# Kernel optimization log

Measured on AMD Instinct MI355X. Metric: run time of the kernel, lower is better.

The kernel has to match this reference:

```python
import jax, jax.numpy as jnp
import numpy as np

B, S, D, H, MULT = 4, 2048, 768, 12, 4
HD = D // H
EPS = 1e-6


def _ln(x, g, b):
    mu = jnp.mean(x, axis=-1, keepdims=True)
    var = jnp.var(x, axis=-1, keepdims=True)
    return (x - mu) * jax.lax.rsqrt(var + EPS) * g + b


def setup_inputs() -> dict:
    key = jax.random.key(0)
    ks = jax.random.split(key, 12)
    sd = 0.02
    inp = {
        "x": jax.random.normal(ks[0], (B, S, D), dtype=jnp.float32),
        "mask": jnp.ones((B, 1, 1, S), dtype=jnp.int32),
        "Wq": jax.random.normal(ks[1], (D, D), dtype=jnp.float32) * sd,
        "bq": jnp.zeros((D,), dtype=jnp.float32),
        "Wk": jax.random.normal(ks[2], (D, D), dtype=jnp.float32) * sd,
        "bk": jnp.zeros((D,), dtype=jnp.float32),
        "Wv": jax.random.normal(ks[3], (D, D), dtype=jnp.float32) * sd,
        "bv": jnp.zeros((D,), dtype=jnp.float32),
        "Wo": jax.random.normal(ks[4], (D, D), dtype=jnp.float32) * sd,
        "bo": jnp.zeros((D,), dtype=jnp.float32),
        "W1": jax.random.normal(ks[5], (D, MULT * D), dtype=jnp.float32) * sd,
        "b1": jnp.zeros((MULT * D,), dtype=jnp.float32),
        "W2": jax.random.normal(ks[6], (MULT * D, D), dtype=jnp.float32) * sd,
        "b2": jnp.zeros((D,), dtype=jnp.float32),
        "g1": jnp.ones((D,), dtype=jnp.float32),
        "be1": jnp.zeros((D,), dtype=jnp.float32),
        "g2": jnp.ones((D,), dtype=jnp.float32),
        "be2": jnp.zeros((D,), dtype=jnp.float32),
    }
    return inp


def reference(x, mask, Wq, bq, Wk, bk, Wv, bv, Wo, bo, W1, b1, W2, b2, g1, be1, g2, be2):
    scale = HD ** -0.5
    # projections -> [B,H,S,HD]
    q = (x @ Wq + bq).reshape(B, S, H, HD).transpose(0, 2, 1, 3)
    k = (x @ Wk + bk).reshape(B, S, H, HD).transpose(0, 2, 1, 3)
    v = (x @ Wv + bv).reshape(B, S, H, HD).transpose(0, 2, 1, 3)
    scores = jnp.einsum("bhqd,bhkd->bhqk", q, k) * scale
    scores = jnp.where(mask == 0, -jnp.inf, scores)
    attn = jax.nn.softmax(scores, axis=-1)
    out = jnp.einsum("bhqk,bhkd->bhqd", attn, v)
    out = out.transpose(0, 2, 1, 3).reshape(B, S, D)
    mha = out @ Wo + bo
    # residual + LN
    h = _ln(mha + x, g1, be1)
    # FFN (dropout inactive in eval; GELU exact as torch nn.GELU default)
    ff = jax.nn.gelu(h @ W1 + b1, approximate=False) @ W2 + b2
    return _ln(ff + h, g2, be2)
```

## Files before the change

kernel.cpp:

```cpp
#include <hip/hip_runtime.h>
#include <hip/hip_bf16.h>
#include <math.h>

#define B_  4
#define S_  2048
#define D_  768
#define H_  12
#define HD_ 64
#define DF_ 3072
#define BS_ (B_*S_)

#define QSCALE 0.18033688011112042f

typedef __attribute__((ext_vector_type(8))) short short8;
typedef __attribute__((ext_vector_type(4))) float f32x4;
typedef __attribute__((ext_vector_type(4))) int  int4v;

__device__ __forceinline__ unsigned short f2b(float f){
    unsigned int x = __float_as_uint(f);
    return (unsigned short)((x + 0x7fffu + ((x >> 16) & 1u)) >> 16);
}
__device__ __forceinline__ float b2f(unsigned short u){
    return __uint_as_float(((unsigned int)u) << 16);
}

typedef __attribute__((address_space(1))) void gvoid_t;
typedef __attribute__((address_space(3))) void lvoid_t;
__device__ __forceinline__ void gload_lds16(const unsigned short* g, unsigned short* l){
    __builtin_amdgcn_global_load_lds((gvoid_t*)g, (lvoid_t*)l, 16, 0, 0);
}

__global__ __launch_bounds__(256) void prep_kernel(
    const float* __restrict__ x,
    const float* __restrict__ Wq, const float* __restrict__ Wk,
    const float* __restrict__ Wv, const float* __restrict__ Wo,
    const float* __restrict__ W1, const float* __restrict__ W2,
    const float* __restrict__ bq, const float* __restrict__ bk, const float* __restrict__ bv,
    unsigned short* __restrict__ xb, unsigned short* __restrict__ wqkvT,
    unsigned short* __restrict__ woT, unsigned short* __restrict__ w1T,
    unsigned short* __restrict__ w2T, float* __restrict__ bqkv)
{
    const int NCVT = (BS_*D_)/256;
    int bid = blockIdx.x;
    if (bid < NCVT){
        int i = bid*256 + threadIdx.x;
        xb[i] = f2b(x[i]);
        return;
    }
    bid -= NCVT;
    __shared__ float t[32][33];
    const float* src; unsigned short* dst; int K, N, bx, by;
    if (bid < 4*576){
        int wsel = bid / 576, tt = bid % 576;
        bx = tt % 24; by = tt / 24; K = D_; N = D_;
        src = (wsel==0)?Wq:(wsel==1)?Wk:(wsel==2)?Wv:Wo;
        dst = (wsel<3) ? (wqkvT + (size_t)wsel*D_*D_) : woT;
    } else if (bid < 4*576 + 2304){
        int tt = bid - 4*576; bx = tt % 96; by = tt / 96; K = D_; N = DF_; src = W1; dst = w1T;
    } else if (bid < 4*576 + 2*2304){
        int tt = bid - 4*576 - 2304; bx = tt % 24; by = tt / 24; K = DF_; N = D_; src = W2; dst = w2T;
    } else {
        int i = (bid - (4*576 + 2*2304))*256 + threadIdx.x;
        if (i < 3*D_) bqkv[i] = (i < D_) ? bq[i] : (i < 2*D_) ? bk[i-D_] : bv[i-2*D_];
        return;
    }
    int tx = threadIdx.x & 31, ty = threadIdx.x >> 5;
    #pragma unroll
    for (int i = 0; i < 4; ++i)
        t[ty + i*8][tx] = src[(size_t)(by*32 + ty + i*8) * N + bx*32 + tx];
    __syncthreads();
    #pragma unroll
    for (int i = 0; i < 4; ++i)
        dst[(size_t)(bx*32 + ty + i*8) * K + by*32 + tx] = f2b(t[tx][ty + i*8]);
}

__global__ __launch_bounds__(256, 3) void gemm_tn(
    const unsigned short* __restrict__ A,
    const unsigned short* __restrict__ Bt,
    const float* __restrict__ bias,
    float* __restrict__ Cf,
    unsigned short* __restrict__ Cb,
    unsigned short* __restrict__ vtg,
    int M, int N, int K, int klen, int act)
{
    __shared__ __align__(16) unsigned short As[128*64];
    __shared__ __align__(16) unsigned short Bs[128*64];

    const int tid  = threadIdx.x;
    const int bm   = blockIdx.y, bn = blockIdx.x, bz = blockIdx.z;
    const int w    = tid >> 6, lane = tid & 63;
    const int l16  = lane & 15, quad = lane >> 4;
    const int wm   = (w >> 1) * 64, wn = (w & 1) * 64;
    const int kbeg = bz * klen;

    const unsigned short* Abase = A  + (size_t)bm * 128 * K;
    const unsigned short* Bbase = Bt + (size_t)bn * 128 * K;

    f32x4 acc[4][4] = {};

    for (int kt = kbeg; kt < kbeg + klen; kt += 64){
        #pragma unroll
        for (int c0 = 0; c0 < 4; ++c0){
            int c = tid + c0 * 256;
            int row = c >> 3, q = c & 7;
            int sw = (q ^ row) & 7;
            gload_lds16(Abase + (size_t)row * K + kt + sw*8, As + c*8);
            gload_lds16(Bbase + (size_t)row * K + kt + sw*8, Bs + c*8);
        }
        __syncthreads();

        #pragma unroll
        for (int kc = 0; kc < 2; ++kc){
            short8 af[4], bf[4];
            #pragma unroll
            for (int mi = 0; mi < 4; ++mi)
                af[mi] = *(const short8*)&As[(wm + mi*16 + l16)*64 + (((kc*4 + quad) ^ l16) & 7)*8];
            #pragma unroll
            for (int ni = 0; ni < 4; ++ni)
                bf[ni] = *(const short8*)&Bs[(wn + ni*16 + l16)*64 + (((kc*4 + quad) ^ l16) & 7)*8];
            #pragma unroll
            for (int mi = 0; mi < 4; ++mi)
                #pragma unroll
                for (int ni = 0; ni < 4; ++ni)
                    acc[mi][ni] = __builtin_amdgcn_mfma_f32_16x16x32_bf16(af[mi], bf[ni], acc[mi][ni], 0, 0, 0);
        }
        __syncthreads();
    }

    if (act == 2 && bn >= 12){
        #pragma unroll
        for (int mi = 0; mi < 4; ++mi){
            int rowbase = bm*128 + wm + mi*16 + quad*4;
            int bidx = rowbase >> 11, s0 = rowbase & 2047;
            int sp = (s0 & ~31) | (((s0 >> 2) & 3) << 3) | (((s0 >> 4) & 1) << 2);
            #pragma unroll
            for (int ni = 0; ni < 4; ++ni){
                int col  = bn*128 + wn + ni*16 + l16;
                int hcol = col - 2*D_;
                int hh   = hcol >> 6, dd = hcol & 63;
                float bia = bias ? bias[col] : 0.f;
                unsigned long long pk = 0;
                #pragma unroll
                for (int r = 0; r < 4; ++r)
                    pk |= (unsigned long long)f2b(acc[mi][ni][r] + bia) << (16*r);
                *(unsigned long long*)(vtg + (((size_t)bidx*H_ + hh)*64 + dd)*2048 + sp) = pk;
            }
        }
        return;
    }

    float* Cfz = Cf ? (Cf + (size_t)bz * M * N) : nullptr;
    const bool addb = (bias != nullptr) && (bz == 0);
    #pragma unroll
    for (int mi = 0; mi < 4; ++mi){
        #pragma unroll
        for (int ni = 0; ni < 4; ++ni){
            int col = bn*128 + wn + ni*16 + l16;
            float bia = addb ? bias[col] : 0.f;
            #pragma unroll
            for (int r = 0; r < 4; ++r){
                int row = bm*128 + wm + mi*16 + quad*4 + r;
                float v = acc[mi][ni][r] + bia;
                if (act == 1){
                    float u = v * (0.7978845608028654f + 0.0356774081f * v * v);
                    float e = __builtin_amdgcn_exp2f(u * 2.885390081777927f);
                    v = 0.5f * v * (1.f + (1.f - 2.f / (e + 1.f)));
                } else if (act == 2 && col < D_) v *= QSCALE;
                size_t idx = (size_t)row * N + col;
                if (Cfz) Cfz[idx] = v;
                if (Cb) Cb[idx] = f2b(v);
            }
        }
    }
}

__global__ __launch_bounds__(512, 6) void attn_kernel(
    const unsigned short* __restrict__ qkv,
    const unsigned short* __restrict__ vtg,
    const int* __restrict__ mask,
    unsigned short* __restrict__ ctx)
{
    __shared__ __align__(16) unsigned short Kl[128*64];
    __shared__ __align__(16) unsigned short Vt[64*128];

    const int tid = threadIdx.x;
    const int bid = blockIdx.x;
    const int hid = bid % 48;
    const int qb  = bid / 48;
    const int h   = hid % H_;
    const int b   = hid / H_;
    const int w   = tid >> 6, lane = tid & 63;
    const int l16 = lane & 15, quad = lane >> 4;
    const int q0  = qb * 128 + w * 16;
    const size_t base = (size_t)b * S_;
    const int hoff = h * HD_;

    short8 qf[2];
    #pragma unroll
    for (int kc = 0; kc < 2; ++kc)
        qf[kc] = *(const short8*)(qkv + (base + q0 + l16)*2304 + hoff + kc*32 + quad*8);

    f32x4 o[4] = {};
    float l_s = 0.f;

    const unsigned short* vrow = vtg + ((size_t)(b*H_ + h) * 64) * 2048;

    for (int kt = 0; kt < S_/128; ++kt){
        __syncthreads();
        #pragma unroll
        for (int c0 = 0; c0 < 2; ++c0){
            int c = tid + c0*512;
            int rr = c >> 3, ch = c & 7;
            int sw = (ch ^ rr) & 7;
            gload_lds16(qkv + (base + kt*128 + rr)*2304 + D_ + hoff + sw*8, Kl + c*8);
            int d = c >> 4, pch = c & 15;
            int lch = (pch ^ d) & 15;
            gload_lds16(vrow + (size_t)d*2048 + kt*128 + lch*8, Vt + c*8);
        }
        __syncthreads();

        int mv0 = mask[b*S_ + kt*128 + lane];
        int mv1 = mask[b*S_ + kt*128 + 64 + lane];
        const bool allok = __all((mv0 != 0) && (mv1 != 0));

        #pragma unroll
        for (int t = 0; t < 4; ++t){
            f32x4 sf2[2] = {};
            #pragma unroll
            for (int kc = 0; kc < 2; ++kc){
                int co = (((kc*4 + quad) ^ l16) & 7)*8;
                short8 k0 = *(const short8*)&Kl[((2*t  )*16 + l16)*64 + co];
                short8 k1 = *(const short8*)&Kl[((2*t+1)*16 + l16)*64 + co];
                sf2[0] = __builtin_amdgcn_mfma_f32_16x16x32_bf16(k0, qf[kc], sf2[0], 0, 0, 0);
                sf2[1] = __builtin_amdgcn_mfma_f32_16x16x32_bf16(k1, qf[kc], sf2[1], 0, 0, 0);
            }
            if (!allok){
                #pragma unroll
                for (int j = 0; j < 2; ++j)
                    #pragma unroll
                    for (int r = 0; r < 4; ++r)
                        if (mask[b*S_ + kt*128 + (2*t+j)*16 + quad*4 + r] == 0)
                            sf2[j][r] = -1e30f;
            }
            #pragma unroll
            for (int j = 0; j < 2; ++j)
                #pragma unroll
                for (int r = 0; r < 4; ++r){
                    float p = __builtin_amdgcn_exp2f(sf2[j][r]);
                    sf2[j][r] = p; l_s += p;
                }
            union { unsigned int u[4]; short8 s; } pk;
            pk.u[0] = __builtin_amdgcn_perm(__float_as_uint(sf2[0][1]), __float_as_uint(sf2[0][0]), 0x07060302u);
            pk.u[1] = __builtin_amdgcn_perm(__float_as_uint(sf2[0][3]), __float_as_uint(sf2[0][2]), 0x07060302u);
            pk.u[2] = __builtin_amdgcn_perm(__float_as_uint(sf2[1][1]), __float_as_uint(sf2[1][0]), 0x07060302u);
            pk.u[3] = __builtin_amdgcn_perm(__float_as_uint(sf2[1][3]), __float_as_uint(sf2[1][2]), 0x07060302u);
            #pragma unroll
            for (int nt = 0; nt < 4; ++nt){
                int d = nt*16 + l16;
                short8 vf = *(const short8*)&Vt[d*128 + (((t*4 + quad) ^ l16) & 15)*8];
                o[nt] = __builtin_amdgcn_mfma_f32_16x16x32_bf16(pk.s, vf, o[nt], 0, 0, 0);
            }
        }
    }

    l_s += __shfl_xor(l_s, 16);
    l_s += __shfl_xor(l_s, 32);
    float linv[4];
    #pragma unroll
    for (int r = 0; r < 4; ++r)
        linv[r] = 1.f / __shfl(l_s, quad*4 + r);
    #pragma unroll
    for (int nt = 0; nt < 4; ++nt)
        #pragma unroll
        for (int r = 0; r < 4; ++r){
            int qrow = q0 + quad*4 + r;
            ctx[(base + qrow)*D_ + hoff + nt*16 + l16] = f2b(o[nt][r] * linv[r]);
        }
}

__global__ __launch_bounds__(256) void ln_kernel(
    const float* __restrict__ inp, const float* __restrict__ inp2,
    const float* __restrict__ resf, const unsigned short* __restrict__ resb,
    const float* __restrict__ g, const float* __restrict__ be,
    float* __restrict__ outf, unsigned short* __restrict__ outb)
{
    const int row = blockIdx.x;
    const int tid = threadIdx.x;
    const float* ip = inp + (size_t)row * D_;
    const float* ip2 = inp2 ? inp2 + (size_t)row * D_ : nullptr;

    float v[3], s = 0.f, ss = 0.f;
    #pragma unroll
    for (int i = 0; i < 3; ++i){
        int c = tid + i*256;
        float x = ip[c];
        if (ip2) x += ip2[c];
        x += resf ? resf[(size_t)row * D_ + c] : b2f(resb[(size_t)row * D_ + c]);
        v[i] = x; s += x; ss += x * x;
    }
    #pragma unroll
    for (int d = 1; d < 64; d <<= 1){ s += __shfl_xor(s, d); ss += __shfl_xor(ss, d); }
    __shared__ float rs[4], rss[4];
    int w = tid >> 6;
    if ((tid & 63) == 0){ rs[w] = s; rss[w] = ss; }
    __syncthreads();
    s  = rs[0] + rs[1] + rs[2] + rs[3];
    ss = rss[0] + rss[1] + rss[2] + rss[3];
    float mu   = s * (1.f / 768.f);
    float var  = ss * (1.f / 768.f) - mu * mu;
    float rstd = rsqrtf(var + 1e-6f);
    #pragma unroll
    for (int i = 0; i < 3; ++i){
        int c = tid + i*256;
        float y = (v[i] - mu) * rstd * g[c] + be[c];
        if (outf) outf[(size_t)row * D_ + c] = y;
        if (outb) outb[(size_t)row * D_ + c] = f2b(y);
    }
}

extern "C" void kernel_launch(void* const* d_in, const int* in_sizes, int n_in,
                              void* d_out, int out_size, void* d_ws, size_t ws_size,
                              hipStream_t stream)
{
    const float* x    = (const float*)d_in[0];
    const int*   mask = (const int*)  d_in[1];
    const float* Wq   = (const float*)d_in[2];
    const float* bq   = (const float*)d_in[3];
    const float* Wk   = (const float*)d_in[4];
    const float* bk   = (const float*)d_in[5];
    const float* Wv   = (const float*)d_in[6];
    const float* bv   = (const float*)d_in[7];
    const float* Wo   = (const float*)d_in[8];
    const float* bo   = (const float*)d_in[9];
    const float* W1   = (const float*)d_in[10];
    const float* b1   = (const float*)d_in[11];
    const float* W2   = (const float*)d_in[12];
    const float* b2   = (const float*)d_in[13];
    const float* g1   = (const float*)d_in[14];
    const float* be1  = (const float*)d_in[15];
    const float* g2   = (const float*)d_in[16];
    const float* be2  = (const float*)d_in[17];
    float* out = (float*)d_out;
    (void)in_sizes; (void)n_in; (void)out_size; (void)ws_size;

    char* ws = (char*)d_ws;
    const size_t n_x = (size_t)BS_ * D_;

    size_t off = 0;
    auto take = [&](size_t bytes){ size_t o = off; off += (bytes + 255) & ~(size_t)255; return o; };
    unsigned short* xb    = (unsigned short*)(ws + take(n_x * 2));
    unsigned short* hb    = xb;
    unsigned short* wqkvT = (unsigned short*)(ws + take((size_t)3*D_*D_ * 2));
    unsigned short* woT   = (unsigned short*)(ws + take((size_t)D_*D_ * 2));
    unsigned short* w1T   = (unsigned short*)(ws + take((size_t)D_*DF_ * 2));
    unsigned short* w2T   = (unsigned short*)(ws + take((size_t)D_*DF_ * 2));
    float*          bqkv  = (float*)(ws + take((size_t)3*D_ * 4));
    size_t big = take((size_t)BS_ * 2304 * 2 + n_x * 2);
    unsigned short* qkvb = (unsigned short*)(ws + big);
    unsigned short* ctxb = qkvb + (size_t)BS_ * 2304;
    unsigned short* ff1b = qkvb;
    float* pf32 = (float*)(ws + take(2 * n_x * 4));
    float* mhaf = pf32;
    float* ff2f = pf32;
    unsigned short* vtg = (unsigned short*)(ws + take(n_x * 2));

    prep_kernel<<<24576 + 3*2304 + 9, 256, 0, stream>>>(
        x, Wq, Wk, Wv, Wo, W1, W2, bq, bk, bv,
        xb, wqkvT, woT, w1T, w2T, bqkv);

    dim3 blk(256);
    gemm_tn<<<dim3(18, 64, 1), blk, 0, stream>>>(xb, wqkvT, bqkv, nullptr, qkvb, vtg, BS_, 3*D_, D_, D_, 2);
    attn_kernel<<<B_ * H_ * (S_/128), 512, 0, stream>>>(qkvb, vtg, mask, ctxb);
    gemm_tn<<<dim3(6, 64, 2), blk, 0, stream>>>(ctxb, woT, bo, mhaf, nullptr, nullptr, BS_, D_, D_, D_/2, 0);
    ln_kernel<<<BS_, blk, 0, stream>>>(mhaf, mhaf + n_x, x, nullptr, g1, be1, nullptr, hb);
    gemm_tn<<<dim3(24, 64, 1), blk, 0, stream>>>(hb, w1T, b1, nullptr, ff1b, nullptr, BS_, DF_, D_, D_, 1);
    gemm_tn<<<dim3(6, 64, 2), blk, 0, stream>>>(ff1b, w2T, b2, ff2f, nullptr, nullptr, BS_, D_, DF_, DF_/2, 0);
    ln_kernel<<<BS_, blk, 0, stream>>>(ff2f, ff2f + n_x, nullptr, hb, g2, be2, out, nullptr);
}
```

Measured before the change: 421.5 us.

## Rewrite GEMM as 256x256 tiles with double-buffered LDS and ping-pong MFMA scheduling

```diff
diff --git a/kernel.cpp b/kernel.cpp
--- a/kernel.cpp
+++ b/kernel.cpp
@@ -14,7 +14,6 @@
 
 typedef __attribute__((ext_vector_type(8))) short short8;
 typedef __attribute__((ext_vector_type(4))) float f32x4;
-typedef __attribute__((ext_vector_type(4))) int  int4v;
 
 __device__ __forceinline__ unsigned short f2b(float f){
     unsigned int x = __float_as_uint(f);
@@ -74,7 +73,7 @@
         dst[(size_t)(bx*32 + ty + i*8) * K + by*32 + tx] = f2b(t[tx][ty + i*8]);
 }
 
-__global__ __launch_bounds__(256, 3) void gemm_tn(
+__global__ __launch_bounds__(512, 2) void gemm_tn(
     const unsigned short* __restrict__ A,
     const unsigned short* __restrict__ Bt,
     const float* __restrict__ bias,
@@ -83,66 +82,133 @@
     unsigned short* __restrict__ vtg,
     int M, int N, int K, int klen, int act)
 {
-    __shared__ __align__(16) unsigned short As[128*64];
-    __shared__ __align__(16) unsigned short Bs[128*64];
+    __shared__ __align__(16) unsigned short Asl[2*2*8192];
+    __shared__ __align__(16) unsigned short Bsl[2*2*8192];
 
     const int tid  = threadIdx.x;
-    const int bm   = blockIdx.y, bn = blockIdx.x, bz = blockIdx.z;
-    const int w    = tid >> 6, lane = tid & 63;
+    const int lane = tid & 63, w = tid >> 6;
     const int l16  = lane & 15, quad = lane >> 4;
-    const int wm   = (w >> 1) * 64, wn = (w & 1) * 64;
+    const int wr   = w >> 2, wc = w & 3;
+
+    int nwg = gridDim.x * gridDim.y;
+    int wg  = blockIdx.y * gridDim.x + blockIdx.x;
+    if ((nwg & 7) == 0) wg = (wg & 7) * (nwg >> 3) + (wg >> 3);
+    const int bn = wg % gridDim.x, bm = wg / gridDim.x;
+    const int bz = blockIdx.z;
     const int kbeg = bz * klen;
-
-    const unsigned short* Abase = A  + (size_t)bm * 128 * K;
-    const unsigned short* Bbase = Bt + (size_t)bn * 128 * K;
-
-    f32x4 acc[4][4] = {};
-
-    for (int kt = kbeg; kt < kbeg + klen; kt += 64){
-        #pragma unroll
-        for (int c0 = 0; c0 < 4; ++c0){
-            int c = tid + c0 * 256;
-            int row = c >> 3, q = c & 7;
-            int sw = (q ^ row) & 7;
-            gload_lds16(Abase + (size_t)row * K + kt + sw*8, As + c*8);
-            gload_lds16(Bbase + (size_t)row * K + kt + sw*8, Bs + c*8);
-        }
-        __syncthreads();
-
-        #pragma unroll
-        for (int kc = 0; kc < 2; ++kc){
-            short8 af[4], bf[4];
-            #pragma unroll
-            for (int mi = 0; mi < 4; ++mi)
-                af[mi] = *(const short8*)&As[(wm + mi*16 + l16)*64 + (((kc*4 + quad) ^ l16) & 7)*8];
-            #pragma unroll
-            for (int ni = 0; ni < 4; ++ni)
-                bf[ni] = *(const short8*)&Bs[(wn + ni*16 + l16)*64 + (((kc*4 + quad) ^ l16) & 7)*8];
-            #pragma unroll
-            for (int mi = 0; mi < 4; ++mi)
-                #pragma unroll
-                for (int ni = 0; ni < 4; ++ni)
-                    acc[mi][ni] = __builtin_amdgcn_mfma_f32_16x16x32_bf16(af[mi], bf[ni], acc[mi][ni], 0, 0, 0);
-        }
-        __syncthreads();
-    }
-
-    if (act == 2 && bn >= 12){
-        #pragma unroll
-        for (int mi = 0; mi < 4; ++mi){
-            int rowbase = bm*128 + wm + mi*16 + quad*4;
+    const int T = klen >> 6;
+
+    const unsigned short* Abase = A  + (size_t)bm * 256 * K;
+    const unsigned short* Bbase = Bt + (size_t)bn * 256 * K;
+
+    const int c0l = tid >> 3, c0q = tid & 7;
+    const int sw0 = (c0q ^ c0l) & 7;
+    const int aro0 = (2*c0l + (sw0 >> 2)) * K + (sw0 & 3) * 8;
+    const int aro1 = aro0 + 128 * K;
+    const int ld0  = tid * 8, ld1 = tid * 8 + 4096;
+
+#define STG(_t, isB, kc) do{ \
+    const int _tc = ((_t) < T) ? (_t) : (T-1); \
+    const unsigned short* gb = (isB) ? Bbase : Abase; \
+    unsigned short* lb = ((isB) ? Bsl : Asl) + ((((_t)&1)<<1)|(kc))*8192; \
+    const int ko = kbeg + _tc*64 + (kc)*32; \
+    gload_lds16(gb + aro0 + ko, lb + ld0); \
+    gload_lds16(gb + aro1 + ko, lb + ld1); \
+}while(0)
+
+    const int qa  = ((l16 & 1) << 2) | quad;
+    const int aL0 = wr*64 + (l16 >> 1);
+    const int bL0 = wc*32 + (l16 >> 1);
+
+#define LDF(h, L) (*(const short8*)((h) + (L)*64 + (((qa) ^ (L)) & 7)*8))
+
+#define MM16(MB) \
+    _Pragma("unroll") \
+    for (int mi = 0; mi < 4; ++mi){ \
+      _Pragma("unroll") \
+      for (int nj = 0; nj < 4; ++nj) \
+        acc[(MB)+mi][nj] = __builtin_amdgcn_mfma_f32_16x16x32_bf16(af[mi], bf[nj], acc[(MB)+mi][nj], 0, 0, 0); \
+    }
+
+    f32x4 acc[8][4] = {};
+
+    STG(0,0,0); STG(0,0,1); STG(0,1,0); STG(0,1,1); STG(1,0,0); STG(1,1,0);
+    asm volatile("s_waitcnt vmcnt(4)" ::: "memory");
+    __builtin_amdgcn_sched_barrier(0);
+    __builtin_amdgcn_s_barrier();
+
+    for (int t = 0; t < T; ++t){
+        const unsigned short* Ah0 = Asl + (((t&1)<<1)|0)*8192;
+        const unsigned short* Ah1 = Asl + (((t&1)<<1)|1)*8192;
+        const unsigned short* Bh0 = Bsl + (((t&1)<<1)|0)*8192;
+        const unsigned short* Bh1 = Bsl + (((t&1)<<1)|1)*8192;
+        short8 af[4], bf[4];
+
+        #pragma unroll
+        for (int mi = 0; mi < 4; ++mi) af[mi] = LDF(Ah0, aL0 + mi*8);
+        #pragma unroll
+        for (int nj = 0; nj < 4; ++nj) bf[nj] = LDF(Bh0, bL0 + nj*8);
+        STG(t+1, 0, 1);
+        __builtin_amdgcn_s_barrier();
+        __builtin_amdgcn_s_setprio(1);
+        MM16(0)
+        __builtin_amdgcn_s_setprio(0);
+        __builtin_amdgcn_s_barrier();
+
+        #pragma unroll
+        for (int mi = 0; mi < 4; ++mi) af[mi] = LDF(Ah0, aL0 + 32 + mi*8);
+        STG(t+1, 1, 1);
+        asm volatile("s_waitcnt vmcnt(6)" ::: "memory");
+        __builtin_amdgcn_sched_barrier(0);
+        __builtin_amdgcn_s_barrier();
+        __builtin_amdgcn_s_setprio(1);
+        MM16(4)
+        __builtin_amdgcn_s_setprio(0);
+        __builtin_amdgcn_s_barrier();
+
+        #pragma unroll
+        for (int mi = 0; mi < 4; ++mi) af[mi] = LDF(Ah1, aL0 + mi*8);
+        #pragma unroll
+        for (int nj = 0; nj < 4; ++nj) bf[nj] = LDF(Bh1, bL0 + nj*8);
+        STG(t+2, 0, 0);
+        __builtin_amdgcn_s_barrier();
+        __builtin_amdgcn_s_setprio(1);
+        MM16(0)
+        __builtin_amdgcn_s_setprio(0);
+        __builtin_amdgcn_s_barrier();
+
+        #pragma unroll
+        for (int mi = 0; mi < 4; ++mi) af[mi] = LDF(Ah1, aL0 + 32 + mi*8);
+        STG(t+2, 1, 0);
+        asm volatile("s_waitcnt vmcnt(6)" ::: "memory");
+        __builtin_amdgcn_sched_barrier(0);
+        __builtin_amdgcn_s_barrier();
+        __builtin_amdgcn_s_setprio(1);
+        MM16(4)
+        __builtin_amdgcn_s_setprio(0);
+        __builtin_amdgcn_s_barrier();
+    }
+
+#undef STG
+#undef LDF
+#undef MM16
+
+    if (act == 2 && bn >= 6){
+        #pragma unroll
+        for (int mi = 0; mi < 8; ++mi){
+            int rowbase = bm*256 + wr*128 + mi*16 + quad*4;
             int bidx = rowbase >> 11, s0 = rowbase & 2047;
             int sp = (s0 & ~31) | (((s0 >> 2) & 3) << 3) | (((s0 >> 4) & 1) << 2);
             #pragma unroll
-            for (int ni = 0; ni < 4; ++ni){
-                int col  = bn*128 + wn + ni*16 + l16;
+            for (int nj = 0; nj < 4; ++nj){
+                int col  = bn*256 + wc*64 + nj*16 + l16;
                 int hcol = col - 2*D_;
                 int hh   = hcol >> 6, dd = hcol & 63;
                 float bia = bias ? bias[col] : 0.f;
                 unsigned long long pk = 0;
                 #pragma unroll
                 for (int r = 0; r < 4; ++r)
-                    pk |= (unsigned long long)f2b(acc[mi][ni][r] + bia) << (16*r);
+                    pk |= (unsigned long long)f2b(acc[mi][nj][r] + bia) << (16*r);
                 *(unsigned long long*)(vtg + (((size_t)bidx*H_ + hh)*64 + dd)*2048 + sp) = pk;
             }
         }
@@ -152,15 +218,15 @@
     float* Cfz = Cf ? (Cf + (size_t)bz * M * N) : nullptr;
     const bool addb = (bias != nullptr) && (bz == 0);
     #pragma unroll
-    for (int mi = 0; mi < 4; ++mi){
-        #pragma unroll
-        for (int ni = 0; ni < 4; ++ni){
-            int col = bn*128 + wn + ni*16 + l16;
+    for (int mi = 0; mi < 8; ++mi){
+        #pragma unroll
+        for (int nj = 0; nj < 4; ++nj){
+            int col = bn*256 + wc*64 + nj*16 + l16;
             float bia = addb ? bias[col] : 0.f;
             #pragma unroll
             for (int r = 0; r < 4; ++r){
-                int row = bm*128 + wm + mi*16 + quad*4 + r;
-                float v = acc[mi][ni][r] + bia;
+                int row = bm*256 + wr*128 + mi*16 + quad*4 + r;
+                float v = acc[mi][nj][r] + bia;
                 if (act == 1){
                     float u = v * (0.7978845608028654f + 0.0356774081f * v * v);
                     float e = __builtin_amdgcn_exp2f(u * 2.885390081777927f);
@@ -368,12 +434,12 @@
         x, Wq, Wk, Wv, Wo, W1, W2, bq, bk, bv,
         xb, wqkvT, woT, w1T, w2T, bqkv);
 
-    dim3 blk(256);
-    gemm_tn<<<dim3(18, 64, 1), blk, 0, stream>>>(xb, wqkvT, bqkv, nullptr, qkvb, vtg, BS_, 3*D_, D_, D_, 2);
+    dim3 blk(512);
+    gemm_tn<<<dim3(9, 32, 1), blk, 0, stream>>>(xb, wqkvT, bqkv, nullptr, qkvb, vtg, BS_, 3*D_, D_, D_, 2);
     attn_kernel<<<B_ * H_ * (S_/128), 512, 0, stream>>>(qkvb, vtg, mask, ctxb);
-    gemm_tn<<<dim3(6, 64, 2), blk, 0, stream>>>(ctxb, woT, bo, mhaf, nullptr, nullptr, BS_, D_, D_, D_/2, 0);
-    ln_kernel<<<BS_, blk, 0, stream>>>(mhaf, mhaf + n_x, x, nullptr, g1, be1, nullptr, hb);
-    gemm_tn<<<dim3(24, 64, 1), blk, 0, stream>>>(hb, w1T, b1, nullptr, ff1b, nullptr, BS_, DF_, D_, D_, 1);
-    gemm_tn<<<dim3(6, 64, 2), blk, 0, stream>>>(ff1b, w2T, b2, ff2f, nullptr, nullptr, BS_, D_, DF_, DF_/2, 0);
-    ln_kernel<<<BS_, blk, 0, stream>>>(ff2f, ff2f + n_x, nullptr, hb, g2, be2, out, nullptr);
-}
+    gemm_tn<<<dim3(3, 32, 2), blk, 0, stream>>>(ctxb, woT, bo, mhaf, nullptr, nullptr, BS_, D_, D_, D_/2, 0);
+    ln_kernel<<<BS_, 256, 0, stream>>>(mhaf, mhaf + n_x, x, nullptr, g1, be1, nullptr, hb);
+    gemm_tn<<<dim3(12, 32, 1), blk, 0, stream>>>(hb, w1T, b1, nullptr, ff1b, nullptr, BS_, DF_, D_, D_, 1);
+    gemm_tn<<<dim3(3, 32, 2), blk, 0, stream>>>(ff1b, w2T, b2, ff2f, nullptr, nullptr, BS_, D_, DF_, DF_/2, 0);
+    ln_kernel<<<BS_, 256, 0, stream>>>(ff2f, ff2f + n_x, nullptr, hb, g2, be2, out, nullptr);
+}
```

Result: slower. 459.9 us (+9.1%).
